# Performance work log

Measured on AMD Instinct MI355X. Metric: run time of the kernel, lower is better.

Reference implementation:

```python
import jax, jax.numpy as jnp
import numpy as np

D_MODEL = 2048
NUM_HEADS = 16
D_K = D_MODEL // NUM_HEADS
SEQ = 2048
BATCH = 2
THETA = 10000.0


def setup_inputs() -> dict:
    key = jax.random.key(0)
    ks = jax.random.split(key, 5)
    s = 1.0 / np.sqrt(D_MODEL)
    return {
        "x": jax.random.normal(ks[0], (BATCH, SEQ, D_MODEL), jnp.float32),
        "wq": jax.random.normal(ks[1], (D_MODEL, D_MODEL), jnp.float32) * s,
        "wk": jax.random.normal(ks[2], (D_MODEL, D_MODEL), jnp.float32) * s,
        "wv": jax.random.normal(ks[3], (D_MODEL, D_MODEL), jnp.float32) * s,
        "wo": jax.random.normal(ks[4], (D_MODEL, D_MODEL), jnp.float32) * s,
    }


def _rope_tables(seq_len, d_k, theta, dtype):
    pos = jnp.arange(seq_len, dtype=dtype)[:, None]            # [S,1]
    inv = theta ** (-(jnp.arange(0, d_k, 2, dtype=dtype) / d_k))  # [d_k/2]
    ang = pos * inv                                            # [S, d_k/2]
    sin = jnp.repeat(jnp.sin(ang), 2, axis=1)                  # [S, d_k] interleaved
    cos = jnp.repeat(jnp.cos(ang), 2, axis=1)
    return sin, cos


def _apply_rope(x, sin, cos):
    # x: [..., S, d_k]; interleaved-pair rotation
    xp = x.reshape(x.shape[:-1] + (x.shape[-1] // 2, 2))
    swapped = jnp.stack((-xp[..., 1], xp[..., 0]), axis=-1).reshape(x.shape)
    return x * cos + swapped * sin


def reference(x, wq, wk, wv, wo):
    B, S, D = x.shape
    H, dk = NUM_HEADS, D_K
    # projections: weights are (H*dk, D); q/k/v -> [B,H,S,dk]
    q = jnp.einsum("bsd,hkd->bhsk", x, wq.reshape(H, dk, D))
    k = jnp.einsum("bsd,hkd->bhsk", x, wk.reshape(H, dk, D))
    v = jnp.einsum("bsd,hkd->bhsk", x, wv.reshape(H, dk, D))
    sin, cos = _rope_tables(S, dk, THETA, x.dtype)
    q = _apply_rope(q, sin, cos)
    k = _apply_rope(k, sin, cos)
    scores = jnp.einsum("bhqk,bhsk->bhqs", q, k) / jnp.sqrt(jnp.asarray(dk, x.dtype))
    causal = jnp.triu(jnp.ones((S, S), dtype=bool), k=1)
    scores = jnp.where(causal, -jnp.inf, scores)
    attn = jax.nn.softmax(scores, axis=-1)
    out = jnp.einsum("bhqs,bhsv->bqhv", attn, v).reshape(B, S, H * dk)
    return jnp.einsum("bsf,df->bsd", out, wo)
```

## Files before the change

kernel.cpp:

```cpp
#include <hip/hip_runtime.h>
#include <hip/hip_bf16.h>

#define B_  2
#define S_  2048
#define D_  2048
#define H_  16
#define DK_ 128
#define M_  (B_*S_)

typedef unsigned short u16;
typedef short bf16x8 __attribute__((ext_vector_type(8)));
typedef float f32x4  __attribute__((ext_vector_type(4)));

#define NEG_BIG (-1.0e30f)

__device__ __forceinline__ u16 f2bf(float f){
    unsigned int u = __float_as_uint(f);
    unsigned int r = (u + 0x7fffu + ((u >> 16) & 1u)) >> 16;
    return (u16)r;
}

__device__ __forceinline__ uint4 cvt8(const float* p){
    float4 a = *(const float4*)p;
    float4 b = *(const float4*)(p + 4);
    uint4 r;
    r.x = ((unsigned int)f2bf(a.y) << 16) | (unsigned int)f2bf(a.x);
    r.y = ((unsigned int)f2bf(a.w) << 16) | (unsigned int)f2bf(a.z);
    r.z = ((unsigned int)f2bf(b.y) << 16) | (unsigned int)f2bf(b.x);
    r.w = ((unsigned int)f2bf(b.w) << 16) | (unsigned int)f2bf(b.z);
    return r;
}

__device__ __forceinline__ void unpack8(const uint4 v, float* f){
    f[0]=__uint_as_float(v.x<<16); f[1]=__uint_as_float(v.x&0xffff0000u);
    f[2]=__uint_as_float(v.y<<16); f[3]=__uint_as_float(v.y&0xffff0000u);
    f[4]=__uint_as_float(v.z<<16); f[5]=__uint_as_float(v.z&0xffff0000u);
    f[6]=__uint_as_float(v.w<<16); f[7]=__uint_as_float(v.w&0xffff0000u);
}

__device__ __forceinline__ void async16(const void* g, void* l){
    __builtin_amdgcn_global_load_lds(
        (const __attribute__((address_space(1))) void*)g,
        (__attribute__((address_space(3))) void*)l, 16, 0, 0);
}

__global__ __launch_bounds__(256) void cvt_all(
    const float* __restrict__ x,  const float* __restrict__ wq, const float* __restrict__ wk,
    const float* __restrict__ wv, const float* __restrict__ wo,
    u16* __restrict__ xb, u16* __restrict__ wqb, u16* __restrict__ wkb,
    u16* __restrict__ wvb, u16* __restrict__ wob)
{
    int c = blockIdx.x*256 + threadIdx.x;
    const float* src; u16* dst; int lc;
    if      (c < 1048576){ src = x;  dst = xb;  lc = c; }
    else if (c < 1572864){ src = wq; dst = wqb; lc = c - 1048576; }
    else if (c < 2097152){ src = wk; dst = wkb; lc = c - 1572864; }
    else if (c < 2621440){ src = wv; dst = wvb; lc = c - 2097152; }
    else                 { src = wo; dst = wob; lc = c - 2621440; }
    *(uint4*)&dst[(size_t)lc*8] = cvt8(&src[(size_t)lc*8]);
}

__global__ __launch_bounds__(512, 2) void gemm4ph(
    const u16* __restrict__ A, const u16* __restrict__ W0, const u16* __restrict__ W1,
    u16* __restrict__ C0, u16* __restrict__ C1)
{
    __shared__ __align__(16) u16 Ab[2][256*64];
    __shared__ __align__(16) u16 Bb[2][256*64];

    const int tid  = threadIdx.x;
    const int lane = tid & 63;
    const int w    = tid >> 6;
    const int quad = lane >> 4;
    const int l15  = lane & 15;
    const int wM   = w & 1;
    const int wN   = w >> 1;
    const int bH   = w >> 2;
    const int cw   = w >> 1;
    const int cb   = w & 3;
    const int sw   = l15 & 7;
    const int blockN = blockIdx.x * 256;
    const int blockM = blockIdx.y * 256;

    const u16* Wm = blockIdx.z ? W1 : W0;
    u16*       Cm = blockIdx.z ? C1 : C0;

    f32x4 acc[32];
    #pragma unroll
    for (int i = 0; i < 32; ++i) acc[i] = (f32x4){0.f,0.f,0.f,0.f};

    auto stageA = [&](int t, int l){
        int c  = l*256 + cw*64 + lane;
        int ra = c >> 3, g = c & 7;
        int cl = g ^ (ra & 7);
        int kb = t*64 + cl*8;
        async16(&A[(size_t)(blockM + wM*128 + ra)*2048 + kb],
                &Ab[t & 1][wM*8192 + c*8]);
    };
    auto stageB = [&](int t, int l){
        int c  = l*256 + cb*64 + lane;
        int rb = c >> 3, g = c & 7;
        int cl = g ^ (rb & 7);
        int kb = t*64 + cl*8;
        async16(&Wm[(size_t)(blockN + bH*128 + rb)*2048 + kb],
                &Bb[t & 1][bH*8192 + c*8]);
    };

    stageB(0,0); stageB(0,1); stageB(0,2); stageB(0,3);
    stageA(0,0); stageA(0,1); stageA(0,2); stageA(0,3);
    asm volatile("s_waitcnt vmcnt(2)" ::: "memory");
    __builtin_amdgcn_s_barrier();
    __builtin_amdgcn_sched_barrier(0);

    for (int t = 0; t < 32; ++t){
        const u16* ab = &Ab[t & 1][0];
        const u16* bb = &Bb[t & 1][0];
        const bool st = (t < 31);
        bf16x8 bfv[4][2], af[2][2];

        #pragma unroll
        for (int ni = 0; ni < 4; ++ni)
            #pragma unroll
            for (int kk = 0; kk < 2; ++kk)
                bfv[ni][kk] = *(const bf16x8*)&bb[(wN*64 + ni*16 + l15)*64 + (((kk*4+quad) ^ sw))*8];
        #pragma unroll
        for (int j = 0; j < 2; ++j)
            #pragma unroll
            for (int kk = 0; kk < 2; ++kk)
                af[j][kk] = *(const bf16x8*)&ab[(wM*128 + (0+j)*16 + l15)*64 + (((kk*4+quad) ^ sw))*8];
        if (st){ stageB(t+1, 0); stageB(t+1, 1); }
        __builtin_amdgcn_s_barrier();
        asm volatile("s_waitcnt lgkmcnt(0)" ::: "memory");
        __builtin_amdgcn_sched_barrier(0);
        __builtin_amdgcn_s_setprio(1);
        #pragma unroll
        for (int j = 0; j < 2; ++j)
            #pragma unroll
            for (int ni = 0; ni < 4; ++ni)
                #pragma unroll
                for (int kk = 0; kk < 2; ++kk)
                    acc[(0+j)*4 + ni] = __builtin_amdgcn_mfma_f32_16x16x32_bf16(
                        af[j][kk], bfv[ni][kk], acc[(0+j)*4 + ni], 0, 0, 0);
        __builtin_amdgcn_s_setprio(0);
        __builtin_amdgcn_s_barrier();
        __builtin_amdgcn_sched_barrier(0);

        #pragma unroll
        for (int j = 0; j < 2; ++j)
            #pragma unroll
            for (int kk = 0; kk < 2; ++kk)
                af[j][kk] = *(const bf16x8*)&ab[(wM*128 + (2+j)*16 + l15)*64 + (((kk*4+quad) ^ sw))*8];
        if (st){ stageB(t+1, 2); stageB(t+1, 3); }
        __builtin_amdgcn_s_barrier();
        asm volatile("s_waitcnt lgkmcnt(0)" ::: "memory");
        __builtin_amdgcn_sched_barrier(0);
        __builtin_amdgcn_s_setprio(1);
        #pragma unroll
        for (int j = 0; j < 2; ++j)
            #pragma unroll
            for (int ni = 0; ni < 4; ++ni)
                #pragma unroll
                for (int kk = 0; kk < 2; ++kk)
                    acc[(2+j)*4 + ni] = __builtin_amdgcn_mfma_f32_16x16x32_bf16(
                        af[j][kk], bfv[ni][kk], acc[(2+j)*4 + ni], 0, 0, 0);
        __builtin_amdgcn_s_setprio(0);
        if (st) { asm volatile("s_waitcnt vmcnt(4)" ::: "memory"); }
        else    { asm volatile("s_waitcnt vmcnt(0)" ::: "memory"); }
        __builtin_amdgcn_s_barrier();
        __builtin_amdgcn_sched_barrier(0);

        #pragma unroll
        for (int j = 0; j < 2; ++j)
            #pragma unroll
            for (int kk = 0; kk < 2; ++kk)
                af[j][kk] = *(const bf16x8*)&ab[(wM*128 + (4+j)*16 + l15)*64 + (((kk*4+quad) ^ sw))*8];
        if (st){ stageA(t+1, 0); stageA(t+1, 1); }
        __builtin_amdgcn_s_barrier();
        asm volatile("s_waitcnt lgkmcnt(0)" ::: "memory");
        __builtin_amdgcn_sched_barrier(0);
        __builtin_amdgcn_s_setprio(1);
        #pragma unroll
        for (int j = 0; j < 2; ++j)
            #pragma unroll
            for (int ni = 0; ni < 4; ++ni)
                #pragma unroll
                for (int kk = 0; kk < 2; ++kk)
                    acc[(4+j)*4 + ni] = __builtin_amdgcn_mfma_f32_16x16x32_bf16(
                        af[j][kk], bfv[ni][kk], acc[(4+j)*4 + ni], 0, 0, 0);
        __builtin_amdgcn_s_setprio(0);
        __builtin_amdgcn_s_barrier();
        __builtin_amdgcn_sched_barrier(0);

        #pragma unroll
        for (int j = 0; j < 2; ++j)
            #pragma unroll
            for (int kk = 0; kk < 2; ++kk)
                af[j][kk] = *(const bf16x8*)&ab[(wM*128 + (6+j)*16 + l15)*64 + (((kk*4+quad) ^ sw))*8];
        if (st){ stageA(t+1, 2); stageA(t+1, 3); }
        __builtin_amdgcn_s_barrier();
        asm volatile("s_waitcnt lgkmcnt(0)" ::: "memory");
        __builtin_amdgcn_sched_barrier(0);
        __builtin_amdgcn_s_setprio(1);
        #pragma unroll
        for (int j = 0; j < 2; ++j)
            #pragma unroll
            for (int ni = 0; ni < 4; ++ni)
                #pragma unroll
                for (int kk = 0; kk < 2; ++kk)
                    acc[(6+j)*4 + ni] = __builtin_amdgcn_mfma_f32_16x16x32_bf16(
                        af[j][kk], bfv[ni][kk], acc[(6+j)*4 + ni], 0, 0, 0);
        __builtin_amdgcn_s_setprio(0);
        if (st) { asm volatile("s_waitcnt vmcnt(2)" ::: "memory"); }
        __builtin_amdgcn_s_barrier();
        __builtin_amdgcn_sched_barrier(0);
    }

    const float osc  = blockIdx.z ? 1.0f : 0.12751743f;
    const float nl2t = -13.287712379549449f / 64.0f;
    #pragma unroll
    for (int mi = 0; mi < 8; ++mi){
        #pragma unroll
        for (int ni = 0; ni < 4; ++ni){
            #pragma unroll
            for (int r = 0; r < 4; ++r){
                float v = acc[mi*4 + ni][r];
                int row = blockM + wM*128 + mi*16 + quad*4 + r;
                int col = blockN + wN*64 + ni*16 + l15;
                float pv = __shfl_xor(v, 1, 64);
                int ii = (col >> 1) & 63;
                float inv = exp2f((float)ii * nl2t);
                float ang = (float)(row & 2047) * inv;
                float sn, cn; __sincosf(ang, &sn, &cn);
                float rv = ((col & 1) ? (v*cn + pv*sn) : (v*cn - pv*sn)) * osc;
                int b = row >> 11, s2 = row & 2047;
                int h = col >> 7,  kk = col & 127;
                Cm[(((size_t)(b*H_ + h))*S_ + s2)*DK_ + kk] = f2bf(rv);
            }
        }
    }
}

template<int MODE, int NF>
__global__ __launch_bounds__(512, 2) void gemm256(
    const u16* __restrict__ A, const u16* __restrict__ W0, const u16* __restrict__ W1,
    void* __restrict__ C0, void* __restrict__ C1)
{
    constexpr int BN = NF * 64;
    __shared__ __align__(16) u16 ring[4][(256 + BN) * 32];

    const int tid  = threadIdx.x;
    const int lane = tid & 63;
    const int w    = tid >> 6;
    const int quad = lane >> 4;
    const int l15  = lane & 15;
    const int wM   = w & 1;
    const int wN   = w >> 1;
    const int blockN = blockIdx.x * BN;
    const int blockM = blockIdx.y * 256;

    const u16* Wm; void* Cm;
    if (MODE == 0){ Wm = blockIdx.z ? W1 : W0; Cm = blockIdx.z ? (void*)C1 : (void*)C0; }
    else          { Wm = W0; Cm = C0; }

    const int cswz = quad ^ ((l15 >> 1) & 3);

    f32x4 acc[8 * NF];
    #pragma unroll
    for (int i = 0; i < 8 * NF; ++i) acc[i] = (f32x4){0.f,0.f,0.f,0.f};

    auto stage = [&](int t){
        const int k0 = t * 32;
        u16* la = (u16*)&ring[t & 3][0];
        u16* lb = la + 256*32;
        #pragma unroll
        for (int it = 0; it < 2; ++it){
            int cc  = it*512 + tid;
            int row = cc >> 2;
            int g   = (cc & 3) ^ ((cc >> 3) & 3);
            int kb  = k0 + g*8;
            const u16* ga;
            if (MODE == 1){
                int rg = blockM + row;
                int b = rg >> 11, s2 = rg & 2047;
                int h = kb >> 7,  kk = kb & 127;
                ga = &A[(((size_t)(b*H_ + h))*S_ + s2)*DK_ + kk];
            } else {
                ga = &A[(size_t)(blockM + row)*2048 + kb];
            }
            async16(ga, la + cc*8);
        }
        #pragma unroll
        for (int it = 0; it < BN/128; ++it){
            int cc  = it*512 + tid;
            int row = cc >> 2;
            int g   = (cc & 3) ^ ((cc >> 3) & 3);
            int kb  = k0 + g*8;
            async16(&Wm[(size_t)(blockN + row)*2048 + kb], lb + cc*8);
        }
    };

    stage(0); stage(1); stage(2);
    if constexpr (NF == 4) asm volatile("s_waitcnt vmcnt(8)" ::: "memory");
    else                   asm volatile("s_waitcnt vmcnt(6)" ::: "memory");
    __builtin_amdgcn_s_barrier();
    __builtin_amdgcn_sched_barrier(0);

    for (int t = 0; t < 64; ++t){
        const u16* la = (const u16*)&ring[t & 3][0];
        const u16* lb = la + 256*32;

        if (t <= 60) stage(t + 3);

        bf16x8 bfv[NF];
        #pragma unroll
        for (int ni = 0; ni < NF; ++ni)
            bfv[ni] = *(const bf16x8*)&lb[(wN*(NF*16) + ni*16 + l15)*32 + cswz*8];

        #pragma unroll
        for (int hf = 0; hf < 2; ++hf){
            bf16x8 af[4];
            #pragma unroll
            for (int mi = 0; mi < 4; ++mi)
                af[mi] = *(const bf16x8*)&la[(wM*128 + hf*64 + mi*16 + l15)*32 + cswz*8];
            __builtin_amdgcn_s_setprio(1);
            #pragma unroll
            for (int mi = 0; mi < 4; ++mi)
                #pragma unroll
                for (int ni = 0; ni < NF; ++ni)
                    acc[(hf*4 + mi)*NF + ni] = __builtin_amdgcn_mfma_f32_16x16x32_bf16(
                        af[mi], bfv[ni], acc[(hf*4 + mi)*NF + ni], 0, 0, 0);
            __builtin_amdgcn_s_setprio(0);
        }

        if constexpr (NF == 4){
            if (t <= 60)      { asm volatile("s_waitcnt vmcnt(8)" ::: "memory"); }
            else if (t == 61) { asm volatile("s_waitcnt vmcnt(4)" ::: "memory"); }
            else if (t == 62) { asm volatile("s_waitcnt vmcnt(0)" ::: "memory"); }
        } else {
            if (t <= 60)      { asm volatile("s_waitcnt vmcnt(6)" ::: "memory"); }
            else if (t == 61) { asm volatile("s_waitcnt vmcnt(3)" ::: "memory"); }
            else if (t == 62) { asm volatile("s_waitcnt vmcnt(0)" ::: "memory"); }
        }
        __builtin_amdgcn_s_barrier();
        __builtin_amdgcn_sched_barrier(0);
    }

    #pragma unroll
    for (int hf = 0; hf < 2; ++hf){
        #pragma unroll
        for (int mi = 0; mi < 4; ++mi){
            #pragma unroll
            for (int ni = 0; ni < NF; ++ni){
                #pragma unroll
                for (int r = 0; r < 4; ++r){
                    float v = acc[(hf*4 + mi)*NF + ni][r];
                    int row = blockM + wM*128 + hf*64 + mi*16 + quad*4 + r;
                    int col = blockN + wN*(NF*16) + ni*16 + l15;
                    if (MODE == 0){
                        int b = row >> 11, s2 = row & 2047;
                        int h = col >> 7,  kk = col & 127;
                        ((u16*)Cm)[(((size_t)(b*H_ + h))*S_ + s2)*DK_ + kk] = f2bf(v);
                    } else if (MODE == 2){
                        int h = row >> 7,  kk = row & 127;
                        int b = col >> 11, s2 = col & 2047;
                        ((u16*)Cm)[(((size_t)(b*H_ + h))*DK_ + kk)*S_ + s2] = f2bf(v);
                    } else {
                        ((float*)Cm)[(size_t)row*2048 + col] = v;
                    }
                }
            }
        }
    }
}

template<int MODE>
__global__ __launch_bounds__(256) void gemm_bt(
    const void* __restrict__ Av,
    const float* __restrict__ W0, const float* __restrict__ W1,
    void* __restrict__ C0, void* __restrict__ C1)
{
    __shared__ u16 As[128*40];
    __shared__ u16 Bs[128*40];

    const int tid  = threadIdx.x;
    const int lane = tid & 63;
    const int w    = tid >> 6;
    const int quad = lane >> 4;
    const int l15  = lane & 15;
    const int blockN = blockIdx.x * 128;
    const int blockM = blockIdx.y * 128;

    const float* Wm; void* Cm;
    if (MODE == 0){ Wm = blockIdx.z ? W1 : W0; Cm = blockIdx.z ? (void*)C1 : (void*)C0; }
    else          { Wm = W0; Cm = C0; }

    const int waveM = (w & 1) * 64;
    const int waveN = (w >> 1) * 64;

    f32x4 acc[16];
    #pragma unroll
    for (int i = 0; i < 16; ++i) acc[i] = (f32x4){0.f,0.f,0.f,0.f};

    for (int k0 = 0; k0 < 2048; k0 += 32){
        __syncthreads();
        #pragma unroll
        for (int it = 0; it < 2; ++it){
            int cc  = tid + it*256;
            int row = cc >> 2;
            int ch  = cc & 3;
            int kb  = k0 + ch*8;
            uint4 va;
            if (MODE == 1){
                int g = blockM + row;
                int b = g >> 11, s2 = g & 2047;
                int h = kb >> 7, kk = kb & 127;
                va = *(const uint4*)&((const u16*)Av)[(((size_t)(b*H_ + h))*S_ + s2)*DK_ + kk];
            } else {
                va = cvt8(&((const float*)Av)[(size_t)(blockM+row)*2048 + kb]);
            }
            uint4 vb = cvt8(&Wm[(size_t)(blockN+row)*2048 + kb]);
            *(uint4*)&As[row*40 + ch*8] = va;
            *(uint4*)&Bs[row*40 + ch*8] = vb;
        }
        __syncthreads();

        bf16x8 af[4], bfv[4];
        #pragma unroll
        for (int mi = 0; mi < 4; ++mi)
            af[mi]  = *(const bf16x8*)&As[(waveM + mi*16 + l15)*40 + quad*8];
        #pragma unroll
        for (int ni = 0; ni < 4; ++ni)
            bfv[ni] = *(const bf16x8*)&Bs[(waveN + ni*16 + l15)*40 + quad*8];
        #pragma unroll
        for (int mi = 0; mi < 4; ++mi)
            #pragma unroll
            for (int ni = 0; ni < 4; ++ni)
                acc[mi*4+ni] = __builtin_amdgcn_mfma_f32_16x16x32_bf16(
                                   af[mi], bfv[ni], acc[mi*4+ni], 0, 0, 0);
    }

    #pragma unroll
    for (int mi = 0; mi < 4; ++mi){
        #pragma unroll
        for (int ni = 0; ni < 4; ++ni){
            #pragma unroll
            for (int r = 0; r < 4; ++r){
                float v = acc[mi*4+ni][r];
                int row = blockM + waveM + mi*16 + quad*4 + r;
                int col = blockN + waveN + ni*16 + l15;
                if (MODE == 0){
                    int b = row >> 11, s2 = row & 2047;
                    int h = col >> 7,  kk = col & 127;
                    ((u16*)Cm)[(((size_t)(b*H_ + h))*S_ + s2)*DK_ + kk] = f2bf(v);
                } else if (MODE == 2){
                    int h = row >> 7,  kk = row & 127;
                    int b = col >> 11, s2 = col & 2047;
                    ((u16*)Cm)[(((size_t)(b*H_ + h))*DK_ + kk)*S_ + s2] = f2bf(v);
                } else {
                    ((float*)Cm)[(size_t)row*2048 + col] = v;
                }
            }
        }
    }
}

__global__ __launch_bounds__(256) void rope_kernel(u16* __restrict__ Q, u16* __restrict__ K)
{
    u16* T = blockIdx.y ? K : Q;
    const float osc = blockIdx.y ? 1.0f : 0.12751743f;
    int t  = blockIdx.x * 256 + threadIdx.x;
    int i0 = (t & 15) * 4;
    int s  = (t >> 4) & 2047;
    size_t base = ((size_t)(t >> 4)) * 128 + (size_t)i0 * 2;
    uint4 v = *(const uint4*)&T[base];
    float f[8]; unpack8(v, f);
    const float nl2t = -13.287712379549449f / 64.0f;
    float sf = (float)s;
    unsigned int out[4];
    #pragma unroll
    for (int p = 0; p < 4; ++p){
        float inv = exp2f((float)(i0 + p) * nl2t);
        float ang = sf * inv;
        float sn, cn;
        sincosf(ang, &sn, &cn);
        float e0 = f[2*p], e1 = f[2*p+1];
        float r0 = (e0*cn - e1*sn) * osc;
        float r1 = (e1*cn + e0*sn) * osc;
        out[p] = ((unsigned int)f2bf(r1) << 16) | (unsigned int)f2bf(r0);
    }
    uint4 ov; ov.x = out[0]; ov.y = out[1]; ov.z = out[2]; ov.w = out[3];
    *(uint4*)&T[base] = ov;
}

__global__ __launch_bounds__(256, 2) void attn_mfma(
    const u16* Q, const u16* __restrict__ K,
    const u16* __restrict__ VT, u16* O)
{
    __shared__ __align__(16) u16 Ks[2][64*128];
    __shared__ __align__(16) u16 Vs[2][128*64];
    __shared__ __align__(16) u16 Ps[4][32*64];

    const int tid  = threadIdx.x;
    const int bh   = blockIdx.x;
    const int qb   = (int)gridDim.y - 1 - (int)blockIdx.y;
    const int w    = tid >> 6;
    const int lane = tid & 63;
    const int quad = lane >> 4;
    const int l15  = lane & 15;
    const int sw   = l15 & 7;
    const size_t qkb = (size_t)bh * S_ * DK_;

    const int qw = qb*128 + w*32;

    bf16x8 aq[2][4];
    #pragma unroll
    for (int mt = 0; mt < 2; ++mt){
        const u16* qp = &Q[qkb + (size_t)(qw + mt*16 + l15)*128 + quad*8];
        #pragma unroll
        for (int kt = 0; kt < 4; ++kt)
            aq[mt][kt] = *(const bf16x8*)(qp + kt*32);
    }

    f32x4 oa[2][8];
    float l_i[2] = {0.f, 0.f};
    #pragma unroll
    for (int mt = 0; mt < 2; ++mt)
        #pragma unroll
        for (int vt = 0; vt < 8; ++vt) oa[mt][vt] = (f32x4){0.f,0.f,0.f,0.f};

    auto stage = [&](int kb, int buf){
        #pragma unroll
        for (int it = 0; it < 4; ++it){
            int cc  = tid + it*256;
            int row = cc >> 4, cl = cc & 15;
            async16(&K[qkb + (size_t)(kb*64 + row)*128 + (size_t)((cl ^ (row & 7))*8)],
                    &Ks[buf][cc*8]);
        }
        #pragma unroll
        for (int it = 0; it < 4; ++it){
            int cc  = tid + it*256;
            int row = cc >> 3, cl = cc & 7;
            async16(&VT[qkb + (size_t)row*S_ + (size_t)(kb*64 + (cl ^ (row & 7))*8)],
                    &Vs[buf][cc*8]);
        }
    };

    const int nkb = 2*qb + 2;
    stage(0, 0);
    __syncthreads();

    for (int kb = 0; kb < nkb; ++kb){
        const int cur = kb & 1;
        if (kb + 1 < nkb) stage(kb + 1, cur ^ 1);

        if (kb*64 <= qw + 31){
            const u16* ks = &Ks[cur][0];
            const u16* vs = &Vs[cur][0];

            f32x4 s[2][4];
            __builtin_amdgcn_s_setprio(1);
            #pragma unroll
            for (int nt = 0; nt < 4; ++nt){
                bf16x8 ak[4];
                #pragma unroll
                for (int kt = 0; kt < 4; ++kt)
                    ak[kt] = *(const bf16x8*)&ks[(nt*16 + l15)*128 + ((kt*4 + quad) ^ sw)*8];
                #pragma unroll
                for (int mt = 0; mt < 2; ++mt){
                    f32x4 a = (f32x4){0.f,0.f,0.f,0.f};
                    #pragma unroll
                    for (int kt = 0; kt < 4; ++kt)
                        a = __builtin_amdgcn_mfma_f32_16x16x32_bf16(ak[kt], aq[mt][kt], a, 0,0,0);
                    s[mt][nt] = a;
                }
            }
            __builtin_amdgcn_s_setprio(0);

            if (kb*64 + 63 > qw){
                #pragma unroll
                for (int mt = 0; mt < 2; ++mt){
                    int qg = qw + mt*16 + l15;
                    #pragma unroll
                    for (int nt = 0; nt < 4; ++nt)
                        #pragma unroll
                        for (int rr = 0; rr < 4; ++rr){
                            int jg = kb*64 + nt*16 + quad*4 + rr;
                            if (jg > qg) s[mt][nt][rr] = NEG_BIG;
                        }
                }
            }

            #pragma unroll
            for (int mt = 0; mt < 2; ++mt){
                float ps = 0.f;
                #pragma unroll
                for (int nt = 0; nt < 4; ++nt)
                    #pragma unroll
                    for (int rr = 0; rr < 4; ++rr){
                        float p = exp2f(s[mt][nt][rr] - 16.0f);
                        s[mt][nt][rr] = p; ps += p;
                    }
                ps += __shfl_xor(ps, 16, 64);
                ps += __shfl_xor(ps, 32, 64);
                l_i[mt] += ps;
            }

            u16* pw = Ps[w];
            #pragma unroll
            for (int mt = 0; mt < 2; ++mt)
              #pragma unroll
              for (int nt = 0; nt < 4; ++nt){
                  uint2 pk;
                  asm("v_cvt_pk_bf16_f32 %0, %1, %2" : "=v"(pk.x) : "v"(s[mt][nt][0]), "v"(s[mt][nt][1]));
                  asm("v_cvt_pk_bf16_f32 %0, %1, %2" : "=v"(pk.y) : "v"(s[mt][nt][2]), "v"(s[mt][nt][3]));
                  int c = (nt*2 + (quad >> 1)) ^ sw;
                  *(uint2*)&pw[(mt*16 + l15)*64 + c*8 + (quad & 1)*4] = pk;
              }

            bf16x8 pa[2][2];
            #pragma unroll
            for (int mt = 0; mt < 2; ++mt)
              #pragma unroll
              for (int kt = 0; kt < 2; ++kt)
                pa[mt][kt] = *(const bf16x8*)&pw[(mt*16 + l15)*64 + ((kt*4 + quad) ^ sw)*8];

            __builtin_amdgcn_s_setprio(1);
            #pragma unroll
            for (int vt = 0; vt < 8; ++vt){
                bf16x8 bv[2];
                #pragma unroll
                for (int kt = 0; kt < 2; ++kt)
                    bv[kt] = *(const bf16x8*)&vs[(vt*16 + l15)*64 + ((kt*4 + quad) ^ sw)*8];
                #pragma unroll
                for (int mt = 0; mt < 2; ++mt)
                  #pragma unroll
                  for (int kt = 0; kt < 2; ++kt)
                    oa[mt][vt] = __builtin_amdgcn_mfma_f32_16x16x32_bf16(
                                     pa[mt][kt], bv[kt], oa[mt][vt], 0,0,0);
            }
            __builtin_amdgcn_s_setprio(0);
        }

        __syncthreads();
    }

    #pragma unroll
    for (int mt = 0; mt < 2; ++mt){
        #pragma unroll
        for (int rr = 0; rr < 4; ++rr){
            float lv = __shfl(l_i[mt], (lane & 48) | (quad*4 + rr), 64);
            float inv = 1.f / lv;
            int qg = qw + mt*16 + quad*4 + rr;
            #pragma unroll
            for (int vt = 0; vt < 8; ++vt)
                O[qkb + (size_t)qg*128 + vt*16 + l15] = f2bf(oa[mt][vt][rr] * inv);
        }
    }
}

extern "C" void kernel_launch(void* const* d_in, const int* in_sizes, int n_in,
                              void* d_out, int out_size, void* d_ws, size_t ws_size,
                              hipStream_t stream)
{
    const float* x  = (const float*)d_in[0];
    const float* wq = (const float*)d_in[1];
    const float* wk = (const float*)d_in[2];
    const float* wv = (const float*)d_in[3];
    const float* wo = (const float*)d_in[4];
    float* out = (float*)d_out;

    const size_t NT = (size_t)B_ * H_ * S_ * DK_;
    const size_t NW = (size_t)D_ * D_;

    if (ws_size >= (size_t)50331648){
        u16* Qw  = (u16*)d_ws;
        u16* Kw  = Qw + NT;
        u16* wvb = Qw + 2*NT;
        u16* wob = wvb + NW;
        u16* xb  = (u16*)d_out;
        u16* wqb = xb + NT;
        u16* wkb = wqb + NW;
        u16* VT  = xb + NT;
        u16* Ow  = Qw;

        cvt_all<<<dim3(12288), 256, 0, stream>>>(x, wq, wk, wv, wo,
                                                 xb, wqb, wkb, wvb, wob);
        gemm4ph<<<dim3(8, 16, 2), 512, 0, stream>>>(xb, wqb, wkb, Qw, Kw);
        gemm256<2,2><<<dim3(32, 8, 1), 512, 0, stream>>>(wvb, xb, nullptr, VT, nullptr);
        attn_mfma<<<dim3(32, 16), 256, 0, stream>>>(Qw, Kw, VT, Ow);
        gemm256<1,2><<<dim3(16, 16, 1), 512, 0, stream>>>(Ow, wob, nullptr, out, nullptr);
    } else {
        u16* Qw  = (u16*)d_ws;
        u16* Vtd = (u16*)d_out;
        u16* Kw  = (u16*)d_out + NT;
        u16* Ow  = Qw;
        gemm_bt<0><<<dim3(16, 32, 2), 256, 0, stream>>>(x, wq, wk, Qw, Kw);
        gemm_bt<2><<<dim3(32, 16, 1), 256, 0, stream>>>(wv, x, nullptr, Vtd, nullptr);
        rope_kernel<<<dim3(4096, 2), 256, 0, stream>>>(Qw, Kw);
        attn_mfma<<<dim3(32, 16), 256, 0, stream>>>(Qw, Kw, Vtd, Ow);
        gemm_bt<1><<<dim3(16, 32, 1), 256, 0, stream>>>(Ow, wo, nullptr, out, nullptr);
    }
}
```

Baseline: 342.0 us.

## Replace 256-row 4-stage GEMM with 128x128 double-buffered async GEMM for V and output projections

Removes the gemm256 kernel (256xBN tiles, 512 threads, 4-deep LDS ring) and adds gemm2ph, a 128x128 tile kernel with 256 threads, an XOR-swizzled LDS layout and two-stage async global-to-LDS loads. The V projection and output projection launches now use it with twice as many blocks and a launch bound allowing three blocks per CU. The aim is better occupancy and load balance across CUs for these GEMMs. In exchange each tile reuses less data, the pipeline is shallower and there are more barriers per K step.

Result: slower. 364.8 us (+6.7%).

```diff
diff --git a/kernel.cpp b/kernel.cpp
--- a/kernel.cpp
+++ b/kernel.cpp
@@ -239,147 +239,13 @@
     }
 }
 
-template<int MODE, int NF>
-__global__ __launch_bounds__(512, 2) void gemm256(
+template<int MODE>
+__global__ __launch_bounds__(256, 3) void gemm2ph(
     const u16* __restrict__ A, const u16* __restrict__ W0, const u16* __restrict__ W1,
     void* __restrict__ C0, void* __restrict__ C1)
 {
-    constexpr int BN = NF * 64;
-    __shared__ __align__(16) u16 ring[4][(256 + BN) * 32];
-
-    const int tid  = threadIdx.x;
-    const int lane = tid & 63;
-    const int w    = tid >> 6;
-    const int quad = lane >> 4;
-    const int l15  = lane & 15;
-    const int wM   = w & 1;
-    const int wN   = w >> 1;
-    const int blockN = blockIdx.x * BN;
-    const int blockM = blockIdx.y * 256;
-
-    const u16* Wm; void* Cm;
-    if (MODE == 0){ Wm = blockIdx.z ? W1 : W0; Cm = blockIdx.z ? (void*)C1 : (void*)C0; }
-    else          { Wm = W0; Cm = C0; }
-
-    const int cswz = quad ^ ((l15 >> 1) & 3);
-
-    f32x4 acc[8 * NF];
-    #pragma unroll
-    for (int i = 0; i < 8 * NF; ++i) acc[i] = (f32x4){0.f,0.f,0.f,0.f};
-
-    auto stage = [&](int t){
-        const int k0 = t * 32;
-        u16* la = (u16*)&ring[t & 3][0];
-        u16* lb = la + 256*32;
-        #pragma unroll
-        for (int it = 0; it < 2; ++it){
-            int cc  = it*512 + tid;
-            int row = cc >> 2;
-            int g   = (cc & 3) ^ ((cc >> 3) & 3);
-            int kb  = k0 + g*8;
-            const u16* ga;
-            if (MODE == 1){
-                int rg = blockM + row;
-                int b = rg >> 11, s2 = rg & 2047;
-                int h = kb >> 7,  kk = kb & 127;
-                ga = &A[(((size_t)(b*H_ + h))*S_ + s2)*DK_ + kk];
-            } else {
-                ga = &A[(size_t)(blockM + row)*2048 + kb];
-            }
-            async16(ga, la + cc*8);
-        }
-        #pragma unroll
-        for (int it = 0; it < BN/128; ++it){
-            int cc  = it*512 + tid;
-            int row = cc >> 2;
-            int g   = (cc & 3) ^ ((cc >> 3) & 3);
-            int kb  = k0 + g*8;
-            async16(&Wm[(size_t)(blockN + row)*2048 + kb], lb + cc*8);
-        }
-    };
-
-    stage(0); stage(1); stage(2);
-    if constexpr (NF == 4) asm volatile("s_waitcnt vmcnt(8)" ::: "memory");
-    else                   asm volatile("s_waitcnt vmcnt(6)" ::: "memory");
-    __builtin_amdgcn_s_barrier();
-    __builtin_amdgcn_sched_barrier(0);
-
-    for (int t = 0; t < 64; ++t){
-        const u16* la = (const u16*)&ring[t & 3][0];
-        const u16* lb = la + 256*32;
-
-        if (t <= 60) stage(t + 3);
-
-        bf16x8 bfv[NF];
-        #pragma unroll
-        for (int ni = 0; ni < NF; ++ni)
-            bfv[ni] = *(const bf16x8*)&lb[(wN*(NF*16) + ni*16 + l15)*32 + cswz*8];
-
-        #pragma unroll
-        for (int hf = 0; hf < 2; ++hf){
-            bf16x8 af[4];
-            #pragma unroll
-            for (int mi = 0; mi < 4; ++mi)
-                af[mi] = *(const bf16x8*)&la[(wM*128 + hf*64 + mi*16 + l15)*32 + cswz*8];
-            __builtin_amdgcn_s_setprio(1);
-            #pragma unroll
-            for (int mi = 0; mi < 4; ++mi)
-                #pragma unroll
-                for (int ni = 0; ni < NF; ++ni)
-                    acc[(hf*4 + mi)*NF + ni] = __builtin_amdgcn_mfma_f32_16x16x32_bf16(
-                        af[mi], bfv[ni], acc[(hf*4 + mi)*NF + ni], 0, 0, 0);
-            __builtin_amdgcn_s_setprio(0);
-        }
-
-        if constexpr (NF == 4){
-            if (t <= 60)      { asm volatile("s_waitcnt vmcnt(8)" ::: "memory"); }
-            else if (t == 61) { asm volatile("s_waitcnt vmcnt(4)" ::: "memory"); }
-            else if (t == 62) { asm volatile("s_waitcnt vmcnt(0)" ::: "memory"); }
-        } else {
-            if (t <= 60)      { asm volatile("s_waitcnt vmcnt(6)" ::: "memory"); }
-            else if (t == 61) { asm volatile("s_waitcnt vmcnt(3)" ::: "memory"); }
-            else if (t == 62) { asm volatile("s_waitcnt vmcnt(0)" ::: "memory"); }
-        }
-        __builtin_amdgcn_s_barrier();
-        __builtin_amdgcn_sched_barrier(0);
-    }
-
-    #pragma unroll
-    for (int hf = 0; hf < 2; ++hf){
-        #pragma unroll
-        for (int mi = 0; mi < 4; ++mi){
-            #pragma unroll
-            for (int ni = 0; ni < NF; ++ni){
-                #pragma unroll
-                for (int r = 0; r < 4; ++r){
-                    float v = acc[(hf*4 + mi)*NF + ni][r];
-                    int row = blockM + wM*128 + hf*64 + mi*16 + quad*4 + r;
-                    int col = blockN + wN*(NF*16) + ni*16 + l15;
-                    if (MODE == 0){
-                        int b = row >> 11, s2 = row & 2047;
-                        int h = col >> 7,  kk = col & 127;
-                        ((u16*)Cm)[(((size_t)(b*H_ + h))*S_ + s2)*DK_ + kk] = f2bf(v);
-                    } else if (MODE == 2){
-                        int h = row >> 7,  kk = row & 127;
-                        int b = col >> 11, s2 = col & 2047;
-                        ((u16*)Cm)[(((size_t)(b*H_ + h))*DK_ + kk)*S_ + s2] = f2bf(v);
-                    } else {
-                        ((float*)Cm)[(size_t)row*2048 + col] = v;
-                    }
-                }
-            }
-        }
-    }
-}
-
-template<int MODE>
-__global__ __launch_bounds__(256) void gemm_bt(
-    const void* __restrict__ Av,
-    const float* __restrict__ W0, const float* __restrict__ W1,
-    void* __restrict__ C0, void* __restrict__ C1)
-{
-    __shared__ u16 As[128*40];
-    __shared__ u16 Bs[128*40];
+    __shared__ __align__(16) u16 As[2][128*32];
+    __shared__ __align__(16) u16 Bs[2][128*32];
 
     const int tid  = threadIdx.x;
     const int lane = tid & 63;
@@ -389,7 +255,7 @@
     const int blockN = blockIdx.x * 128;
     const int blockM = blockIdx.y * 128;
 
-    const float* Wm; void* Cm;
+    const u16* Wm; void* Cm;
     if (MODE == 0){ Wm = blockIdx.z ? W1 : W0; Cm = blockIdx.z ? (void*)C1 : (void*)C0; }
     else          { Wm = W0; Cm = C0; }
 
@@ -400,42 +266,56 @@
     #pragma unroll
     for (int i = 0; i < 16; ++i) acc[i] = (f32x4){0.f,0.f,0.f,0.f};
 
-    for (int k0 = 0; k0 < 2048; k0 += 32){
-        __syncthreads();
+    auto stage = [&](int t, int buf){
+        const int k0 = t * 32;
         #pragma unroll
         for (int it = 0; it < 2; ++it){
             int cc  = tid + it*256;
             int row = cc >> 2;
             int ch  = cc & 3;
-            int kb  = k0 + ch*8;
-            uint4 va;
+            int kb  = k0 + (ch ^ (row & 3))*8;
+            const u16* ga;
             if (MODE == 1){
                 int g = blockM + row;
                 int b = g >> 11, s2 = g & 2047;
                 int h = kb >> 7, kk = kb & 127;
-                va = *(const uint4*)&((const u16*)Av)[(((size_t)(b*H_ + h))*S_ + s2)*DK_ + kk];
+                ga = &A[(((size_t)(b*H_ + h))*S_ + s2)*DK_ + kk];
             } else {
-                va = cvt8(&((const float*)Av)[(size_t)(blockM+row)*2048 + kb]);
-            }
-            uint4 vb = cvt8(&Wm[(size_t)(blockN+row)*2048 + kb]);
-            *(uint4*)&As[row*40 + ch*8] = va;
-            *(uint4*)&Bs[row*40 + ch*8] = vb;
-        }
-        __syncthreads();
+                ga = &A[(size_t)(blockM + row)*2048 + kb];
+            }
+            async16(ga, &As[buf][cc*8]);
+            async16(&Wm[(size_t)(blockN + row)*2048 + kb], &Bs[buf][cc*8]);
+        }
+    };
+
+    stage(0, 0);
+    __syncthreads();
+
+    for (int t = 0; t < 64; ++t){
+        const int cur = t & 1;
+        if (t + 1 < 64) stage(t + 1, cur ^ 1);
 
         bf16x8 af[4], bfv[4];
         #pragma unroll
-        for (int mi = 0; mi < 4; ++mi)
-            af[mi]  = *(const bf16x8*)&As[(waveM + mi*16 + l15)*40 + quad*8];
-        #pragma unroll
-        for (int ni = 0; ni < 4; ++ni)
-            bfv[ni] = *(const bf16x8*)&Bs[(waveN + ni*16 + l15)*40 + quad*8];
+        for (int mi = 0; mi < 4; ++mi){
+            int r = waveM + mi*16 + l15;
+            af[mi]  = *(const bf16x8*)&As[cur][r*32 + (quad ^ (r & 3))*8];
+        }
+        #pragma unroll
+        for (int ni = 0; ni < 4; ++ni){
+            int r = waveN + ni*16 + l15;
+            bfv[ni] = *(const bf16x8*)&Bs[cur][r*32 + (quad ^ (r & 3))*8];
+        }
+        __builtin_amdgcn_s_setprio(1);
         #pragma unroll
         for (int mi = 0; mi < 4; ++mi)
             #pragma unroll
             for (int ni = 0; ni < 4; ++ni)
                 acc[mi*4+ni] = __builtin_amdgcn_mfma_f32_16x16x32_bf16(
                                    af[mi], bfv[ni], acc[mi*4+ni], 0, 0, 0);
+        __builtin_amdgcn_s_setprio(0);
+
+        __syncthreads();
     }
 
     #pragma unroll
@@ -463,6 +343,97 @@
     }
 }
 
+template<int MODE>
+__global__ __launch_bounds__(256) void gemm_bt(
+    const void* __restrict__ Av,
+    const float* __restrict__ W0, const float* __restrict__ W1,
+    void* __restrict__ C0, void* __restrict__ C1)
+{
+    __shared__ u16 As[128*40];
+    __shared__ u16 Bs[128*40];
+
+    const int tid  = threadIdx.x;
+    const int lane = tid & 63;
+    const int w    = tid >> 6;
+    const int quad = lane >> 4;
+    const int l15  = lane & 15;
+    const int blockN = blockIdx.x * 128;
+    const int blockM = blockIdx.y * 128;
+
+    const float* Wm; void* Cm;
+    if (MODE == 0){ Wm = blockIdx.z ? W1 : W0; Cm = blockIdx.z ? (void*)C1 : (void*)C0; }
+    else          { Wm = W0; Cm = C0; }
+
+    const int waveM = (w & 1) * 64;
+    const int waveN = (w >> 1) * 64;
+
+    f32x4 acc[16];
+    #pragma unroll
+    for (int i = 0; i < 16; ++i) acc[i] = (f32x4){0.f,0.f,0.f,0.f};
+
+    for (int k0 = 0; k0 < 2048; k0 += 32){
+        __syncthreads();
+        #pragma unroll
+        for (int it = 0; it < 2; ++it){
+            int cc  = tid + it*256;
+            int row = cc >> 2;
+            int ch  = cc & 3;
+            int kb  = k0 + ch*8;
+            uint4 va;
+            if (MODE == 1){
+                int g = blockM + row;
+                int b = g >> 11, s2 = g & 2047;
+                int h = kb >> 7, kk = kb & 127;
+                va = *(const uint4*)&((const u16*)Av)[(((size_t)(b*H_ + h))*S_ + s2)*DK_ + kk];
+            } else {
+                va = cvt8(&((const float*)Av)[(size_t)(blockM+row)*2048 + kb]);
+            }
+            uint4 vb = cvt8(&Wm[(size_t)(blockN+row)*2048 + kb]);
+            *(uint4*)&As[row*40 + ch*8] = va;
+            *(uint4*)&Bs[row*40 + ch*8] = vb;
+        }
+        __syncthreads();
+
+        bf16x8 af[4], bfv[4];
+        #pragma unroll
+        for (int mi = 0; mi < 4; ++mi)
+            af[mi]  = *(const bf16x8*)&As[(waveM + mi*16 + l15)*40 + quad*8];
+        #pragma unroll
+        for (int ni = 0; ni < 4; ++ni)
+            bfv[ni] = *(const bf16x8*)&Bs[(waveN + ni*16 + l15)*40 + quad*8];
+        #pragma unroll
+        for (int mi = 0; mi < 4; ++mi)
+            #pragma unroll
+            for (int ni = 0; ni < 4; ++ni)
+                acc[mi*4+ni] = __builtin_amdgcn_mfma_f32_16x16x32_bf16(
+                                   af[mi], bfv[ni], acc[mi*4+ni], 0, 0, 0);
+    }
+
+    #pragma unroll
+    for (int mi = 0; mi < 4; ++mi){
+        #pragma unroll
+        for (int ni = 0; ni < 4; ++ni){
+            #pragma unroll
+            for (int r = 0; r < 4; ++r){
+                float v = acc[mi*4+ni][r];
+                int row = blockM + waveM + mi*16 + quad*4 + r;
+                int col = blockN + waveN + ni*16 + l15;
+                if (MODE == 0){
+                    int b = row >> 11, s2 = row & 2047;
+                    int h = col >> 7,  kk = col & 127;
+                    ((u16*)Cm)[(((size_t)(b*H_ + h))*S_ + s2)*DK_ + kk] = f2bf(v);
+                } else if (MODE == 2){
+                    int h = row >> 7,  kk = row & 127;
+                    int b = col >> 11, s2 = col & 2047;
+                    ((u16*)Cm)[(((size_t)(b*H_ + h))*DK_ + kk)*S_ + s2] = f2bf(v);
+                } else {
+                    ((float*)Cm)[(size_t)row*2048 + col] = v;
+                }
+            }
+        }
+    }
+}
+
 __global__ __launch_bounds__(256) void rope_kernel(u16* __restrict__ Q, u16* __restrict__ K)
 {
     u16* T = blockIdx.y ? K : Q;
@@ -685,9 +656,9 @@
         cvt_all<<<dim3(12288), 256, 0, stream>>>(x, wq, wk, wv, wo,
                                                  xb, wqb, wkb, wvb, wob);
         gemm4ph<<<dim3(8, 16, 2), 512, 0, stream>>>(xb, wqb, wkb, Qw, Kw);
-        gemm256<2,2><<<dim3(32, 8, 1), 512, 0, stream>>>(wvb, xb, nullptr, VT, nullptr);
+        gemm2ph<2><<<dim3(32, 16, 1), 256, 0, stream>>>(wvb, xb, nullptr, VT, nullptr);
         attn_mfma<<<dim3(32, 16), 256, 0, stream>>>(Qw, Kw, VT, Ow);
-        gemm256<1,2><<<dim3(16, 16, 1), 512, 0, stream>>>(Ow, wob, nullptr, out, nullptr);
+        gemm2ph<1><<<dim3(16, 32, 1), 256, 0, stream>>>(Ow, wob, nullptr, out, nullptr);
     } else {
         u16* Qw  = (u16*)d_ws;
         u16* Vtd = (u16*)d_out;
```
